# Kernel tuning notes

Hardware: AMD Instinct MI355X
Metric: run time of the kernel (lower is better)

Reference implementation:

```python
import jax, jax.numpy as jnp
import numpy as np

D_MODEL, N_HEADS, D_K, D_V, D_FF, N_LAYERS = 512, 8, 64, 64, 2048, 6
NEG = -1e9
EPS = 1e-5


def layernorm(x):
    # nn.LayerNorm(d_model) created fresh each call: weight=1, bias=0
    mu = jnp.mean(x, axis=-1, keepdims=True)
    var = jnp.var(x, axis=-1, keepdims=True)
    return (x - mu) * jax.lax.rsqrt(var + EPS)


def sinusoidal_pe(seq_len, d_model, dtype=jnp.float32):
    pos = np.arange(seq_len)[:, None].astype(np.float64)
    div = np.exp(np.arange(0, d_model, 2).astype(np.float64) * (-np.log(10000.0) / d_model))
    pe = np.zeros((seq_len, d_model))
    pe[:, 0::2] = np.sin(pos * div)
    pe[:, 1::2] = np.cos(pos * div)
    return jnp.asarray(pe, dtype=dtype)


def mha(q_in, k_in, v_in, mask, Wq, Wk, Wv, Wo):
    # q_in: [B,Lq,D]; k_in/v_in: [B,Lk,D]; mask: [B,Lq,Lk] bool (True = masked)
    B, Lq, _ = q_in.shape
    Lk = k_in.shape[1]
    Q = (q_in @ Wq).reshape(B, Lq, N_HEADS, D_K).transpose(0, 2, 1, 3)
    K = (k_in @ Wk).reshape(B, Lk, N_HEADS, D_K).transpose(0, 2, 1, 3)
    V = (v_in @ Wv).reshape(B, Lk, N_HEADS, D_V).transpose(0, 2, 1, 3)
    scores = jnp.einsum('bhqd,bhkd->bhqk', Q, K) / jnp.sqrt(jnp.asarray(D_K, q_in.dtype))
    scores = jnp.where(mask[:, None, :, :], jnp.asarray(NEG, scores.dtype), scores)
    attn = jax.nn.softmax(scores, axis=-1)
    ctx = jnp.einsum('bhqk,bhkd->bhqd', attn, V)
    ctx = ctx.transpose(0, 2, 1, 3).reshape(B, Lq, N_HEADS * D_V)
    return layernorm(ctx @ Wo + q_in)


def setup_inputs() -> dict:
    key = jax.random.key(0)
    ks = jax.random.split(key, 16)
    B, T, S, V = 8, 1024, 1024, 32000
    s = 0.02
    inp = {
        'dec_inputs': jax.random.randint(ks[0], (B, T), 0, V),
        'enc_inputs': jax.random.randint(ks[1], (B, S), 0, V),
        'enc_outputs': jax.random.normal(ks[2], (B, S, D_MODEL), jnp.float32),
        'emb': jax.random.normal(ks[3], (V, D_MODEL), jnp.float32) * s,
        'Wq_self': jax.random.normal(ks[4], (N_LAYERS, D_MODEL, N_HEADS * D_K), jnp.float32) * s,
        'Wk_self': jax.random.normal(ks[5], (N_LAYERS, D_MODEL, N_HEADS * D_K), jnp.float32) * s,
        'Wv_self': jax.random.normal(ks[6], (N_LAYERS, D_MODEL, N_HEADS * D_V), jnp.float32) * s,
        'Wo_self': jax.random.normal(ks[7], (N_LAYERS, N_HEADS * D_V, D_MODEL), jnp.float32) * s,
        'Wq_cross': jax.random.normal(ks[8], (N_LAYERS, D_MODEL, N_HEADS * D_K), jnp.float32) * s,
        'Wk_cross': jax.random.normal(ks[9], (N_LAYERS, D_MODEL, N_HEADS * D_K), jnp.float32) * s,
        'Wv_cross': jax.random.normal(ks[10], (N_LAYERS, D_MODEL, N_HEADS * D_V), jnp.float32) * s,
        'Wo_cross': jax.random.normal(ks[11], (N_LAYERS, N_HEADS * D_V, D_MODEL), jnp.float32) * s,
        'W1': jax.random.normal(ks[12], (N_LAYERS, D_MODEL, D_FF), jnp.float32) * s,
        'W2': jax.random.normal(ks[13], (N_LAYERS, D_FF, D_MODEL), jnp.float32) * s,
    }
    return inp


def reference(dec_inputs, enc_inputs, enc_outputs, emb, Wq_self, Wk_self, Wv_self, Wo_self,
              Wq_cross, Wk_cross, Wv_cross, Wo_cross, W1, W2):
    B, T = dec_inputs.shape
    S = enc_inputs.shape[1]
    # embedding with padding_idx=0 (row 0 forced to zero)
    emb_eff = emb.at[0].set(0.0)
    x = emb_eff[dec_inputs] + sinusoidal_pe(T, D_MODEL, emb.dtype)[None, :, :]
    # masks: True = masked
    pad_self = (dec_inputs == 0)[:, None, :]                       # [B,1,T]
    causal = jnp.triu(jnp.ones((T, T), bool), k=1)[None, :, :]     # [1,T,T]
    self_mask = pad_self | causal                                  # [B,T,T]
    enc_mask = jnp.broadcast_to((enc_inputs == 0)[:, None, :], (B, T, S))

    def layer(x, p):
        wqs, wks, wvs, wos, wqc, wkc, wvc, woc, w1, w2 = p
        x = mha(x, x, x, self_mask, wqs, wks, wvs, wos)
        x = mha(x, enc_outputs, enc_outputs, enc_mask, wqc, wkc, wvc, woc)
        h = jax.nn.relu(x @ w1) @ w2
        return layernorm(h + x), None

    params = (Wq_self, Wk_self, Wv_self, Wo_self, Wq_cross, Wk_cross, Wv_cross, Wo_cross, W1, W2)
    x, _ = jax.lax.scan(layer, x, params)
    return x
```

## Files before the change

kernel.cpp:

```cpp
#include <hip/hip_runtime.h>
#include <hip/hip_bf16.h>

#define DMODEL 512
#define NH     8
#define DHEAD  64
#define DFF    2048
#define NLAYER 6
#define BB     8
#define TT     1024
#define NTOK   (BB*TT)
#define ACTE   ((size_t)NTOK*DMODEL)

typedef __bf16  bf16x8  __attribute__((ext_vector_type(8)));
typedef float   float4v __attribute__((ext_vector_type(4)));
typedef short   short4v __attribute__((ext_vector_type(4)));
typedef short   short8v __attribute__((ext_vector_type(8)));

__device__ __forceinline__ unsigned short f2bf(float f) {
    __hip_bfloat16 h = __float2bfloat16(f);
    return *reinterpret_cast<unsigned short*>(&h);
}

__device__ __forceinline__ void gl_lds16(const void* g, void* l) {
    __builtin_amdgcn_global_load_lds((const __attribute__((address_space(1))) void*)g,
                                     (__attribute__((address_space(3))) void*)l, 16, 0, 0);
}
__device__ __forceinline__ void wave_order() { __builtin_amdgcn_wave_barrier(); }

struct Tr8Args {
    const float* src[8];
    unsigned short* dst[8];
    int dstL[8];
    int rowOff[8];
};
__global__ __launch_bounds__(256) void transpose8_kernel(Tr8Args a)
{
    __shared__ float tile[64][65];
    const int type = blockIdx.z / 6, lyr = blockIdx.z % 6;
    const float* src = a.src[type] + (size_t)lyr * 512 * 512;
    unsigned short* dst = a.dst[type] + (size_t)lyr * a.dstL[type];
    const int rowOff = a.rowOff[type];
    const int k0 = blockIdx.x * 64, n0 = blockIdx.y * 64;
    const int tid = threadIdx.x;
#pragma unroll
    for (int rep = 0; rep < 16; ++rep) {
        int idx = rep * 256 + tid;
        int r = idx >> 6, c = idx & 63;
        tile[r][c] = src[(size_t)(k0 + r) * 512 + n0 + c];
    }
    __syncthreads();
#pragma unroll
    for (int rep = 0; rep < 16; ++rep) {
        int idx = rep * 256 + tid;
        int r = idx >> 6, c = idx & 63;
        dst[(size_t)(rowOff + n0 + r) * 512 + k0 + c] = f2bf(tile[c][r]);
    }
}

__global__ __launch_bounds__(256) void transpose_conv_kernel(
    const float* __restrict__ W, unsigned short* __restrict__ Wt, int K, int N,
    size_t dstL, int rowOff)
{
    __shared__ float tile[64][65];
    const float* src = W + (size_t)blockIdx.z * K * N;
    unsigned short* dst = Wt + (size_t)blockIdx.z * dstL;
    const int k0 = blockIdx.x * 64, n0 = blockIdx.y * 64;
    const int tid = threadIdx.x;
#pragma unroll
    for (int rep = 0; rep < 16; ++rep) {
        int idx = rep * 256 + tid;
        int r = idx >> 6, c = idx & 63;
        tile[r][c] = src[(size_t)(k0 + r) * N + n0 + c];
    }
    __syncthreads();
#pragma unroll
    for (int rep = 0; rep < 16; ++rep) {
        int idx = rep * 256 + tid;
        int r = idx >> 6, c = idx & 63;
        dst[(size_t)(rowOff + n0 + r) * K + k0 + c] = f2bf(tile[c][r]);
    }
}

__global__ __launch_bounds__(256) void conv_bf16_kernel(
    const float* __restrict__ in, unsigned short* __restrict__ o)
{
    int i = (blockIdx.x * 256 + threadIdx.x) * 4;
    float4v v = *(const float4v*)(in + i);
    short4v w;
    w[0] = (short)f2bf(v[0]); w[1] = (short)f2bf(v[1]);
    w[2] = (short)f2bf(v[2]); w[3] = (short)f2bf(v[3]);
    *(short4v*)(o + i) = w;
}

__global__ __launch_bounds__(256) void embed_kernel(
    const int* __restrict__ dec, const float* __restrict__ emb,
    unsigned short* __restrict__ xb)
{
    const int row = blockIdx.x;
    const int t = row & (TT - 1);
    const int tid = threadIdx.x;
    const int tok = dec[row];
#pragma unroll
    for (int rep = 0; rep < 2; ++rep) {
        int c = tid + rep * 256;
        float e = (tok != 0) ? emb[(size_t)tok * DMODEL + c] : 0.f;
        int j = c >> 1;
        float freq = __expf(-(float)(2 * j) * (9.210340371976184f / 512.f));
        float ang = (float)t * freq;
        float pe = (c & 1) ? cosf(ang) : sinf(ang);
        xb[(size_t)row * DMODEL + c] = f2bf(e + pe);
    }
}

__global__ __launch_bounds__(256) void add_ln2(
    const float* __restrict__ t, unsigned short* __restrict__ xb,
    float* __restrict__ xout)
{
    const int lane = threadIdx.x & 63;
    const int row = blockIdx.x * 4 + (threadIdx.x >> 6);
    const size_t idx = (size_t)row * DMODEL + lane * 8;
    float4v t0 = *(const float4v*)(t + idx);
    float4v t1 = *(const float4v*)(t + idx + 4);
    float4v u0 = *(const float4v*)(t + ACTE + idx);
    float4v u1 = *(const float4v*)(t + ACTE + idx + 4);
    bf16x8 rb = *(const bf16x8*)(xb + idx);
    float v[8];
#pragma unroll
    for (int k = 0; k < 4; ++k) {
        v[k] = t0[k] + u0[k] + (float)rb[k];
        v[4 + k] = t1[k] + u1[k] + (float)rb[4 + k];
    }
    float s = 0.f, sq = 0.f;
#pragma unroll
    for (int k = 0; k < 8; ++k) { s += v[k]; sq += v[k] * v[k]; }
#pragma unroll
    for (int o = 1; o < 64; o <<= 1) { s += __shfl_xor(s, o); sq += __shfl_xor(sq, o); }
    float mu = s * (1.f / 512.f);
    float var = sq * (1.f / 512.f) - mu * mu;
    float rstd = rsqrtf(var + 1e-5f);
    if (xout) {
        float4v y0, y1;
#pragma unroll
        for (int k = 0; k < 4; ++k) { y0[k] = (v[k] - mu) * rstd; y1[k] = (v[4 + k] - mu) * rstd; }
        *(float4v*)(xout + idx) = y0;
        *(float4v*)(xout + idx + 4) = y1;
    } else {
        short8v w;
#pragma unroll
        for (int k = 0; k < 8; ++k) w[k] = (short)f2bf((v[k] - mu) * rstd);
        *(short8v*)(xb + idx) = w;
    }
}

template <int EPI, int SPLITK = 1>
__global__ __launch_bounds__(256) void gemm_bt(
    const unsigned short* __restrict__ A,
    const unsigned short* __restrict__ Bt,
    float* __restrict__ Cf,
    unsigned short* __restrict__ Cb,
    int M, int N, int K)
{
    __shared__ __attribute__((aligned(16))) short As[128 * 32];
    __shared__ __attribute__((aligned(16))) short Bs[128 * 32];
    const int tid = threadIdx.x;
    const int lane = tid & 63, wv = tid >> 6;
    const int quad = lane >> 4, l15 = lane & 15;
    const int m0 = blockIdx.x * 128, n0 = blockIdx.y * 128;
    const int wm = wv & 1, wn = wv >> 1;

    float4v acc[4][4];
#pragma unroll
    for (int i = 0; i < 4; ++i)
#pragma unroll
        for (int j = 0; j < 4; ++j) acc[i][j] = (float4v){0.f, 0.f, 0.f, 0.f};

    const int Kc = K / SPLITK;
    const int kbeg = (SPLITK > 1) ? (int)blockIdx.z * Kc : 0;
    for (int k0 = kbeg; k0 < kbeg + Kc; k0 += 32) {
#pragma unroll
        for (int i = 0; i < 2; ++i) {
            const int inst = wv * 2 + i;
            const int row = inst * 16 + (lane >> 2);
            const int cb = (lane & 3) ^ ((row >> 1) & 3);
            gl_lds16(A + (size_t)(m0 + row) * K + k0 + cb * 8, (char*)As + inst * 1024);
            gl_lds16(Bt + (size_t)(n0 + row) * K + k0 + cb * 8, (char*)Bs + inst * 1024);
        }
        __syncthreads();
        bf16x8 a[4], b[4];
#pragma unroll
        for (int i = 0; i < 4; ++i) {
            const int r = wm * 64 + i * 16 + l15;
            const int st = quad ^ ((r >> 1) & 3);
            a[i] = *(const bf16x8*)&As[r * 32 + st * 8];
        }
#pragma unroll
        for (int j = 0; j < 4; ++j) {
            const int r = wn * 64 + j * 16 + l15;
            const int st = quad ^ ((r >> 1) & 3);
            b[j] = *(const bf16x8*)&Bs[r * 32 + st * 8];
        }
#pragma unroll
        for (int i = 0; i < 4; ++i)
#pragma unroll
            for (int j = 0; j < 4; ++j)
                acc[i][j] = __builtin_amdgcn_mfma_f32_16x16x32_bf16(a[i], b[j], acc[i][j], 0, 0, 0);
        __syncthreads();
    }

    const size_t zoff = (SPLITK > 1) ? (size_t)blockIdx.z * ACTE : 0;
#pragma unroll
    for (int i = 0; i < 4; ++i) {
        const int row_base = m0 + wm * 64 + i * 16 + quad * 4;
#pragma unroll
        for (int j = 0; j < 4; ++j) {
            const int col = n0 + wn * 64 + j * 16 + l15;
#pragma unroll
            for (int r = 0; r < 4; ++r) {
                const int row = row_base + r;
                const float v = acc[i][j][r];
                if (EPI == 0) {
                    Cf[zoff + (size_t)row * N + col] = v;
                } else if (EPI == 1) {
                    Cb[(size_t)row * N + col] = f2bf(fmaxf(v, 0.f));
                } else if (EPI == 2) {
                    const int which = col >> 9;
                    const int b_ = row >> 10, t = row & (TT - 1);
                    const int h = (col >> 6) & 7, d = col & 63;
                    Cb[(size_t)which * ACTE + (((size_t)(b_ * NH + h)) * TT + t) * DHEAD + d] = f2bf(v);
                } else {
                    const int layer = col >> 10, which = (col >> 9) & 1;
                    const int b_ = row >> 10, t = row & (TT - 1);
                    const int h = (col >> 6) & 7, d = col & 63;
                    Cb[(size_t)(layer * 2 + which) * ACTE +
                       (((size_t)(b_ * NH + h)) * TT + t) * DHEAD + d] = f2bf(v);
                }
            }
        }
    }
}

template <bool CAUSAL>
__global__ __launch_bounds__(256) void attn_kernel(
    const unsigned short* __restrict__ Q,
    const unsigned short* __restrict__ Kb,
    const unsigned short* __restrict__ Vb,
    const int* __restrict__ tokens,
    unsigned short* __restrict__ ctx)
{
    __shared__ __attribute__((aligned(16))) short Ks[64 * 64];
    __shared__ __attribute__((aligned(16))) short Vt[64 * 64];
    __shared__ __attribute__((aligned(16))) short Pl[4][16 * 72];
    __shared__ __attribute__((aligned(16))) float alphas[4][16];
    __shared__ int kmask[64];

    const int tid = threadIdx.x, lane = tid & 63, wv = tid >> 6;
    const int quad = lane >> 4, l15 = lane & 15;
    const int p = blockIdx.x;
    const int bh = blockIdx.y;
    const int b = bh >> 3, h = bh & 7;
    const size_t kvbase = (size_t)bh * TT * DHEAD;

    const int qt0 = p;
    const int qt1 = CAUSAL ? (15 - p) : (p + 8);
    const int qg0 = qt0 * 64 + wv * 16 + l15;
    const int qg1 = qt1 * 64 + wv * 16 + l15;

    const bf16x8 qa0 = *(const bf16x8*)&Q[kvbase + (size_t)qg0 * DHEAD + quad * 8];
    const bf16x8 qa1 = *(const bf16x8*)&Q[kvbase + (size_t)qg0 * DHEAD + 32 + quad * 8];
    const bf16x8 qb0 = *(const bf16x8*)&Q[kvbase + (size_t)qg1 * DHEAD + quad * 8];
    const bf16x8 qb1 = *(const bf16x8*)&Q[kvbase + (size_t)qg1 * DHEAD + 32 + quad * 8];

    float4v O0[4], O1[4];
#pragma unroll
    for (int j = 0; j < 4; ++j) { O0[j] = (float4v){0.f,0.f,0.f,0.f}; O1[j] = (float4v){0.f,0.f,0.f,0.f}; }
    float m0_ = -INFINITY, l0_ = 0.f, m1_ = -INFINITY, l1_ = 0.f;

    int kt = 0;
    auto process = [&](const bf16x8& qf0, const bf16x8& qf1, int qg,
                       float& m, float& l, float4v* O) {
        float4v st[4];
#pragma unroll
        for (int i = 0; i < 4; ++i) {
            const int row = i * 16 + l15;
            const int s0 = quad ^ (row & 7);
            const int s1 = (4 + quad) ^ (row & 7);
            bf16x8 kf0 = *(const bf16x8*)&Ks[row * 64 + s0 * 8];
            bf16x8 kf1 = *(const bf16x8*)&Ks[row * 64 + s1 * 8];
            float4v z = (float4v){0.f, 0.f, 0.f, 0.f};
            z = __builtin_amdgcn_mfma_f32_16x16x32_bf16(kf0, qf0, z, 0, 0, 0);
            z = __builtin_amdgcn_mfma_f32_16x16x32_bf16(kf1, qf1, z, 0, 0, 0);
            st[i] = z;
        }
        float sv[16], smax = -INFINITY;
#pragma unroll
        for (int i = 0; i < 4; ++i)
#pragma unroll
            for (int r = 0; r < 4; ++r) {
                const int key_local = i * 16 + quad * 4 + r;
                const int key_g = kt * 64 + key_local;
                bool msk = (kmask[key_local] != 0) || (CAUSAL && key_g > qg);
                float s = msk ? -1e9f : st[i][r] * 0.125f;
                sv[i * 4 + r] = s;
                smax = fmaxf(smax, s);
            }
        smax = fmaxf(smax, __shfl_xor(smax, 16));
        smax = fmaxf(smax, __shfl_xor(smax, 32));
        const float mnew = fmaxf(m, smax);
        const float alpha = __expf(m - mnew);
        float tsum = 0.f;
#pragma unroll
        for (int i = 0; i < 16; ++i) { float pv = __expf(sv[i] - mnew); sv[i] = pv; tsum += pv; }
        tsum += __shfl_xor(tsum, 16);
        tsum += __shfl_xor(tsum, 32);
        l = l * alpha + tsum;
        m = mnew;
        wave_order();
#pragma unroll
        for (int i = 0; i < 4; ++i) {
            short4v pw;
#pragma unroll
            for (int r = 0; r < 4; ++r) pw[r] = (short)f2bf(sv[i * 4 + r]);
            *(short4v*)&Pl[wv][l15 * 72 + i * 16 + quad * 4] = pw;
        }
        if (lane < 16) alphas[wv][lane] = alpha;
        wave_order();
        const float4v aw = *(const float4v*)&alphas[wv][quad * 4];
        const bf16x8 p0 = *(const bf16x8*)&Pl[wv][l15 * 72 + quad * 8];
        const bf16x8 p1 = *(const bf16x8*)&Pl[wv][l15 * 72 + 32 + quad * 8];
#pragma unroll
        for (int j = 0; j < 4; ++j) {
            const int row = j * 16 + l15;
            const int s0 = quad ^ (row & 7);
            const int s1 = (4 + quad) ^ (row & 7);
            bf16x8 v0f = *(const bf16x8*)&Vt[row * 64 + s0 * 8];
            bf16x8 v1f = *(const bf16x8*)&Vt[row * 64 + s1 * 8];
            float4v o = O[j] * aw;
            o = __builtin_amdgcn_mfma_f32_16x16x32_bf16(p0, v0f, o, 0, 0, 0);
            o = __builtin_amdgcn_mfma_f32_16x16x32_bf16(p1, v1f, o, 0, 0, 0);
            O[j] = o;
        }
    };

    const int nkt = CAUSAL ? (qt1 + 1) : 16;
    for (kt = 0; kt < nkt; ++kt) {
        __syncthreads();
#pragma unroll
        for (int i = 0; i < 2; ++i) {
            const int inst = wv * 2 + i;
            const int row = inst * 8 + (lane >> 3);
            const int cb = (lane & 7) ^ (row & 7);
            gl_lds16(Kb + kvbase + (size_t)(kt * 64 + row) * DHEAD + cb * 8,
                     (char*)Ks + inst * 1024);
        }
        {
            const int key0 = (lane & 31) * 2;
            const int d0 = (lane >> 5) * 8 + wv * 16;
            const unsigned short* vp = Vb + kvbase + (size_t)(kt * 64 + key0) * DHEAD + d0;
            short8v r0 = *(const short8v*)vp;
            short8v r1 = *(const short8v*)(vp + DHEAD);
            const int kc = key0 >> 3, ko = key0 & 7;
#pragma unroll
            for (int j = 0; j < 8; ++j) {
                const int d = d0 + j;
                unsigned pk = (unsigned)(unsigned short)r0[j] |
                              ((unsigned)(unsigned short)r1[j] << 16);
                *(unsigned*)&Vt[d * 64 + ((kc ^ (d & 7)) << 3) + ko] = pk;
            }
        }
        if (tid < 64) kmask[tid] = (tokens[(size_t)b * TT + kt * 64 + tid] == 0);
        __syncthreads();

        if (!CAUSAL || kt <= qt0) process(qa0, qa1, qg0, m0_, l0_, O0);
        process(qb0, qb1, qg1, m1_, l1_, O1);
    }

    auto finalize = [&](float l, float4v* O, int qt) {
        wave_order();
        if (lane < 16) alphas[wv][lane] = l;
        wave_order();
        const float4v lw = *(const float4v*)&alphas[wv][quad * 4];
#pragma unroll
        for (int j = 0; j < 4; ++j)
#pragma unroll
            for (int r = 0; r < 4; ++r) {
                const int qrow = qt * 64 + wv * 16 + quad * 4 + r;
                ctx[((size_t)b * TT + qrow) * DMODEL + h * DHEAD + j * 16 + l15] =
                    f2bf(O[j][r] / lw[r]);
            }
    };
    finalize(l0_, O0, qt0);
    finalize(l1_, O1, qt1);
}

extern "C" void kernel_launch(void* const* d_in, const int* in_sizes, int n_in,
                              void* d_out, int out_size, void* d_ws, size_t ws_size,
                              hipStream_t stream)
{
    const int* dec = (const int*)d_in[0];
    const int* enc = (const int*)d_in[1];
    const float* enc_out = (const float*)d_in[2];
    const float* emb = (const float*)d_in[3];
    const float* Wq_s = (const float*)d_in[4];
    const float* Wk_s = (const float*)d_in[5];
    const float* Wv_s = (const float*)d_in[6];
    const float* Wo_s = (const float*)d_in[7];
    const float* Wq_c = (const float*)d_in[8];
    const float* Wk_c = (const float*)d_in[9];
    const float* Wv_c = (const float*)d_in[10];
    const float* Wo_c = (const float*)d_in[11];
    const float* W1 = (const float*)d_in[12];
    const float* W2 = (const float*)d_in[13];
    float* out = (float*)d_out;

    char* p = (char*)d_ws;
    auto carve = [&](size_t bytes) -> char* {
        char* r = p;
        p += (bytes + 255) & ~(size_t)255;
        return r;
    };
    unsigned short* xb   = (unsigned short*)carve(ACTE * 2);
    float* tmp1          = (float*)carve(2 * ACTE * 4);
    unsigned short* qkvb = (unsigned short*)carve(3 * ACTE * 2);
    unsigned short* ctxb = (unsigned short*)carve(ACTE * 2);
    unsigned short* encb = (unsigned short*)carve(ACTE * 2);
    unsigned short* h1   = (unsigned short*)carve((size_t)NTOK * DFF * 2);
    unsigned short* wqkvT = (unsigned short*)carve((size_t)NLAYER * 1536 * 512 * 2);
    unsigned short* woT   = (unsigned short*)carve((size_t)NLAYER * 512 * 512 * 2);
    unsigned short* wqcT  = (unsigned short*)carve((size_t)NLAYER * 512 * 512 * 2);
    unsigned short* wkvcT = (unsigned short*)carve((size_t)NLAYER * 1024 * 512 * 2);
    unsigned short* wocT  = (unsigned short*)carve((size_t)NLAYER * 512 * 512 * 2);
    unsigned short* w1T   = (unsigned short*)carve((size_t)NLAYER * 2048 * 512 * 2);
    unsigned short* w2T   = (unsigned short*)carve((size_t)NLAYER * 512 * 2048 * 2);
    const size_t used = (size_t)(p - (char*)d_ws);
    const bool pre = (used + 12 * ACTE * 2 + 256) <= ws_size;
    unsigned short* KVc = pre ? (unsigned short*)carve(12 * ACTE * 2) : nullptr;

    Tr8Args ta;
    ta.src[0] = Wq_s; ta.dst[0] = wqkvT; ta.dstL[0] = 1536 * 512; ta.rowOff[0] = 0;
    ta.src[1] = Wk_s; ta.dst[1] = wqkvT; ta.dstL[1] = 1536 * 512; ta.rowOff[1] = 512;
    ta.src[2] = Wv_s; ta.dst[2] = wqkvT; ta.dstL[2] = 1536 * 512; ta.rowOff[2] = 1024;
    ta.src[3] = Wo_s; ta.dst[3] = woT;   ta.dstL[3] = 512 * 512;  ta.rowOff[3] = 0;
    ta.src[4] = Wq_c; ta.dst[4] = wqcT;  ta.dstL[4] = 512 * 512;  ta.rowOff[4] = 0;
    ta.src[5] = Wk_c; ta.dst[5] = wkvcT; ta.dstL[5] = 1024 * 512; ta.rowOff[5] = 0;
    ta.src[6] = Wv_c; ta.dst[6] = wkvcT; ta.dstL[6] = 1024 * 512; ta.rowOff[6] = 512;
    ta.src[7] = Wo_c; ta.dst[7] = wocT;  ta.dstL[7] = 512 * 512;  ta.rowOff[7] = 0;
    transpose8_kernel<<<dim3(8, 8, 48), 256, 0, stream>>>(ta);
    transpose_conv_kernel<<<dim3(8, 32, NLAYER), 256, 0, stream>>>(W1, w1T, 512, 2048, (size_t)2048 * 512, 0);
    transpose_conv_kernel<<<dim3(32, 8, NLAYER), 256, 0, stream>>>(W2, w2T, 2048, 512, (size_t)512 * 2048, 0);
    conv_bf16_kernel<<<(int)(ACTE / 1024), 256, 0, stream>>>(enc_out, encb);
    embed_kernel<<<NTOK, 256, 0, stream>>>(dec, emb, xb);

    if (pre)
        gemm_bt<3><<<dim3(64, 48), 256, 0, stream>>>(encb, wkvcT, nullptr, KVc, NTOK, 6144, 512);

    for (int lyr = 0; lyr < NLAYER; ++lyr) {
        const unsigned short* wqkv = wqkvT + (size_t)lyr * 1536 * 512;
        const unsigned short* wo   = woT + (size_t)lyr * 512 * 512;
        const unsigned short* wqc  = wqcT + (size_t)lyr * 512 * 512;
        const unsigned short* wkvc = wkvcT + (size_t)lyr * 1024 * 512;
        const unsigned short* woc  = wocT + (size_t)lyr * 512 * 512;
        const unsigned short* w1   = w1T + (size_t)lyr * 2048 * 512;
        const unsigned short* w2   = w2T + (size_t)lyr * 512 * 2048;

        gemm_bt<2><<<dim3(64, 12), 256, 0, stream>>>(xb, wqkv, nullptr, qkvb, NTOK, 1536, 512);
        attn_kernel<true><<<dim3(8, BB * NH), 256, 0, stream>>>(
            qkvb, qkvb + ACTE, qkvb + 2 * ACTE, dec, ctxb);
        gemm_bt<0, 2><<<dim3(64, 4, 2), 256, 0, stream>>>(ctxb, wo, tmp1, nullptr, NTOK, 512, 512);
        add_ln2<<<NTOK / 4, 256, 0, stream>>>(tmp1, xb, nullptr);

        gemm_bt<2><<<dim3(64, 4), 256, 0, stream>>>(xb, wqc, nullptr, qkvb, NTOK, 512, 512);
        const unsigned short* Kc;
        if (pre) {
            Kc = KVc + (size_t)lyr * 2 * ACTE;
        } else {
            gemm_bt<2><<<dim3(64, 8), 256, 0, stream>>>(encb, wkvc, nullptr, qkvb + ACTE, NTOK, 1024, 512);
            Kc = qkvb + ACTE;
        }
        attn_kernel<false><<<dim3(8, BB * NH), 256, 0, stream>>>(
            qkvb, Kc, Kc + ACTE, enc, ctxb);
        gemm_bt<0, 2><<<dim3(64, 4, 2), 256, 0, stream>>>(ctxb, woc, tmp1, nullptr, NTOK, 512, 512);
        add_ln2<<<NTOK / 4, 256, 0, stream>>>(tmp1, xb, nullptr);

        gemm_bt<1><<<dim3(64, 16), 256, 0, stream>>>(xb, w1, nullptr, h1, NTOK, 2048, 512);
        gemm_bt<0, 2><<<dim3(64, 4, 2), 256, 0, stream>>>(h1, w2, tmp1, nullptr, NTOK, 512, 2048);
        add_ln2<<<NTOK / 4, 256, 0, stream>>>(tmp1, xb, (lyr == NLAYER - 1) ? out : nullptr);
    }
    (void)in_sizes; (void)n_in; (void)out_size;
}
```

Baseline: 1.755 ms.

## Double-buffer K/V tiles in attention and precompute key padding mask via ballot

The attention kernel now double-buffers the K and V LDS tiles. It prefetches the next key tile (K through global_load_lds, V into registers) while the current tile is processed, which cuts the loop to one __syncthreads per iteration instead of two. The padding mask is built with a wave ballot into a 64-bit mask that also folds in the causal mask, replacing per-element shared-memory lookups. The 1/sqrt(d) scale moves into the Q projection epilogue. Dropping the wave barriers around the per-wave P/alpha LDS round-trip relies on in-order LDS access within a wave, and the double buffers increase LDS usage.

```diff
diff --git a/kernel.cpp b/kernel.cpp
--- a/kernel.cpp
+++ b/kernel.cpp
@@ -25,7 +25,6 @@
     __builtin_amdgcn_global_load_lds((const __attribute__((address_space(1))) void*)g,
                                      (__attribute__((address_space(3))) void*)l, 16, 0, 0);
 }
-__device__ __forceinline__ void wave_order() { __builtin_amdgcn_wave_barrier(); }
 
 struct Tr8Args {
     const float* src[8];
@@ -224,9 +223,10 @@
                     Cb[(size_t)row * N + col] = f2bf(fmaxf(v, 0.f));
                 } else if (EPI == 2) {
                     const int which = col >> 9;
+                    const float sc = (which == 0) ? 0.125f : 1.f;
                     const int b_ = row >> 10, t = row & (TT - 1);
                     const int h = (col >> 6) & 7, d = col & 63;
-                    Cb[(size_t)which * ACTE + (((size_t)(b_ * NH + h)) * TT + t) * DHEAD + d] = f2bf(v);
+                    Cb[(size_t)which * ACTE + (((size_t)(b_ * NH + h)) * TT + t) * DHEAD + d] = f2bf(v * sc);
                 } else {
                     const int layer = col >> 10, which = (col >> 9) & 1;
                     const int b_ = row >> 10, t = row & (TT - 1);
@@ -247,11 +247,10 @@
     const int* __restrict__ tokens,
     unsigned short* __restrict__ ctx)
 {
-    __shared__ __attribute__((aligned(16))) short Ks[64 * 64];
-    __shared__ __attribute__((aligned(16))) short Vt[64 * 64];
-    __shared__ __attribute__((aligned(16))) short Pl[4][16 * 72];
-    __shared__ __attribute__((aligned(16))) float alphas[4][16];
-    __shared__ int kmask[64];
+    __shared__ __attribute__((aligned(16))) short Ks[2][64 * 64];
+    __shared__ __attribute__((aligned(16))) short Vt[2][64 * 64];
+    __shared__ __attribute__((aligned(16))) short Pl[2][4][16 * 72];
+    __shared__ __attribute__((aligned(16))) float alph[2][4][16];
 
     const int tid = threadIdx.x, lane = tid & 63, wv = tid >> 6;
     const int quad = lane >> 4, l15 = lane & 15;
@@ -275,31 +274,63 @@
     for (int j = 0; j < 4; ++j) { O0[j] = (float4v){0.f,0.f,0.f,0.f}; O1[j] = (float4v){0.f,0.f,0.f,0.f}; }
     float m0_ = -INFINITY, l0_ = 0.f, m1_ = -INFINITY, l1_ = 0.f;
 
+    const int key0 = (lane & 31) * 2;
+    const int d0 = (lane >> 5) * 8 + wv * 16;
+    auto stageK = [&](int kt, int buf) {
+#pragma unroll
+        for (int i = 0; i < 2; ++i) {
+            const int inst = wv * 2 + i;
+            const int row = inst * 8 + (lane >> 3);
+            const int cb = (lane & 7) ^ (row & 7);
+            gl_lds16(Kb + kvbase + (size_t)(kt * 64 + row) * DHEAD + cb * 8,
+                     (char*)Ks[buf] + inst * 1024);
+        }
+    };
+    auto loadV = [&](int kt, short8v& r0, short8v& r1) {
+        const unsigned short* vp = Vb + kvbase + (size_t)(kt * 64 + key0) * DHEAD + d0;
+        r0 = *(const short8v*)vp;
+        r1 = *(const short8v*)(vp + DHEAD);
+    };
+    auto writeV = [&](int buf, const short8v& r0, const short8v& r1) {
+        const int kc = key0 >> 3, ko = key0 & 7;
+#pragma unroll
+        for (int j = 0; j < 8; ++j) {
+            const int d = d0 + j;
+            unsigned pk = (unsigned)(unsigned short)r0[j] |
+                          ((unsigned)(unsigned short)r1[j] << 16);
+            *(unsigned*)&Vt[buf][d * 64 + ((kc ^ (d & 7)) << 3) + ko] = pk;
+        }
+    };
+
     int kt = 0;
-    auto process = [&](const bf16x8& qf0, const bf16x8& qf1, int qg,
-                       float& m, float& l, float4v* O) {
+    auto process = [&](int ch, const bf16x8& qf0, const bf16x8& qf1, int qg,
+                       float& m, float& l, float4v* O,
+                       int cur, unsigned long long kbits) {
         float4v st[4];
 #pragma unroll
         for (int i = 0; i < 4; ++i) {
             const int row = i * 16 + l15;
             const int s0 = quad ^ (row & 7);
             const int s1 = (4 + quad) ^ (row & 7);
-            bf16x8 kf0 = *(const bf16x8*)&Ks[row * 64 + s0 * 8];
-            bf16x8 kf1 = *(const bf16x8*)&Ks[row * 64 + s1 * 8];
+            bf16x8 kf0 = *(const bf16x8*)&Ks[cur][row * 64 + s0 * 8];
+            bf16x8 kf1 = *(const bf16x8*)&Ks[cur][row * 64 + s1 * 8];
             float4v z = (float4v){0.f, 0.f, 0.f, 0.f};
             z = __builtin_amdgcn_mfma_f32_16x16x32_bf16(kf0, qf0, z, 0, 0, 0);
             z = __builtin_amdgcn_mfma_f32_16x16x32_bf16(kf1, qf1, z, 0, 0, 0);
             st[i] = z;
         }
+        unsigned long long mask = kbits;
+        if (CAUSAL && kt * 64 + 63 > qg) {
+            const int qcol = qg & 63;
+            mask |= (qcol == 63) ? 0ull : (~0ull << (qcol + 1));
+        }
         float sv[16], smax = -INFINITY;
 #pragma unroll
         for (int i = 0; i < 4; ++i)
 #pragma unroll
             for (int r = 0; r < 4; ++r) {
-                const int key_local = i * 16 + quad * 4 + r;
-                const int key_g = kt * 64 + key_local;
-                bool msk = (kmask[key_local] != 0) || (CAUSAL && key_g > qg);
-                float s = msk ? -1e9f : st[i][r] * 0.125f;
+                const int kl = i * 16 + quad * 4 + r;
+                float s = ((mask >> kl) & 1ull) ? -1e9f : st[i][r];
                 sv[i * 4 + r] = s;
                 smax = fmaxf(smax, s);
             }
@@ -314,26 +345,24 @@
         tsum += __shfl_xor(tsum, 32);
         l = l * alpha + tsum;
         m = mnew;
-        wave_order();
 #pragma unroll
         for (int i = 0; i < 4; ++i) {
             short4v pw;
 #pragma unroll
             for (int r = 0; r < 4; ++r) pw[r] = (short)f2bf(sv[i * 4 + r]);
-            *(short4v*)&Pl[wv][l15 * 72 + i * 16 + quad * 4] = pw;
-        }
-        if (lane < 16) alphas[wv][lane] = alpha;
-        wave_order();
-        const float4v aw = *(const float4v*)&alphas[wv][quad * 4];
-        const bf16x8 p0 = *(const bf16x8*)&Pl[wv][l15 * 72 + quad * 8];
-        const bf16x8 p1 = *(const bf16x8*)&Pl[wv][l15 * 72 + 32 + quad * 8];
+            *(short4v*)&Pl[ch][wv][l15 * 72 + i * 16 + quad * 4] = pw;
+        }
+        if (lane < 16) alph[ch][wv][lane] = alpha;
+        const float4v aw = *(const float4v*)&alph[ch][wv][quad * 4];
+        const bf16x8 p0 = *(const bf16x8*)&Pl[ch][wv][l15 * 72 + quad * 8];
+        const bf16x8 p1 = *(const bf16x8*)&Pl[ch][wv][l15 * 72 + 32 + quad * 8];
 #pragma unroll
         for (int j = 0; j < 4; ++j) {
             const int row = j * 16 + l15;
             const int s0 = quad ^ (row & 7);
             const int s1 = (4 + quad) ^ (row & 7);
-            bf16x8 v0f = *(const bf16x8*)&Vt[row * 64 + s0 * 8];
-            bf16x8 v1f = *(const bf16x8*)&Vt[row * 64 + s1 * 8];
+            bf16x8 v0f = *(const bf16x8*)&Vt[cur][row * 64 + s0 * 8];
+            bf16x8 v1f = *(const bf16x8*)&Vt[cur][row * 64 + s1 * 8];
             float4v o = O[j] * aw;
             o = __builtin_amdgcn_mfma_f32_16x16x32_bf16(p0, v0f, o, 0, 0, 0);
             o = __builtin_amdgcn_mfma_f32_16x16x32_bf16(p1, v1f, o, 0, 0, 0);
@@ -342,43 +371,41 @@
     };
 
     const int nkt = CAUSAL ? (qt1 + 1) : 16;
+
+    stageK(0, 0);
+    {
+        short8v v0a, v0b;
+        loadV(0, v0a, v0b);
+        writeV(0, v0a, v0b);
+    }
+    int tok_cur = tokens[(size_t)b * TT + lane];
+    __syncthreads();
+
+    short8v vn0, vn1;
+    int tok_next = 0;
     for (kt = 0; kt < nkt; ++kt) {
+        const int cur = kt & 1, nxt = cur ^ 1;
+        const bool more = (kt + 1 < nkt);
+        if (more) {
+            stageK(kt + 1, nxt);
+            loadV(kt + 1, vn0, vn1);
+            tok_next = tokens[(size_t)b * TT + (kt + 1) * 64 + lane];
+        }
+        const unsigned long long kbits = __ballot(tok_cur == 0);
+
+        if (!CAUSAL || kt <= qt0) process(0, qa0, qa1, qg0, m0_, l0_, O0, cur, kbits);
+        process(1, qb0, qb1, qg1, m1_, l1_, O1, cur, kbits);
+
+        if (more) {
+            writeV(nxt, vn0, vn1);
+            tok_cur = tok_next;
+        }
         __syncthreads();
-#pragma unroll
-        for (int i = 0; i < 2; ++i) {
-            const int inst = wv * 2 + i;
-            const int row = inst * 8 + (lane >> 3);
-            const int cb = (lane & 7) ^ (row & 7);
-            gl_lds16(Kb + kvbase + (size_t)(kt * 64 + row) * DHEAD + cb * 8,
-                     (char*)Ks + inst * 1024);
-        }
-        {
-            const int key0 = (lane & 31) * 2;
-            const int d0 = (lane >> 5) * 8 + wv * 16;
-            const unsigned short* vp = Vb + kvbase + (size_t)(kt * 64 + key0) * DHEAD + d0;
-            short8v r0 = *(const short8v*)vp;
-            short8v r1 = *(const short8v*)(vp + DHEAD);
-            const int kc = key0 >> 3, ko = key0 & 7;
-#pragma unroll
-            for (int j = 0; j < 8; ++j) {
-                const int d = d0 + j;
-                unsigned pk = (unsigned)(unsigned short)r0[j] |
-                              ((unsigned)(unsigned short)r1[j] << 16);
-                *(unsigned*)&Vt[d * 64 + ((kc ^ (d & 7)) << 3) + ko] = pk;
-            }
-        }
-        if (tid < 64) kmask[tid] = (tokens[(size_t)b * TT + kt * 64 + tid] == 0);
-        __syncthreads();
-
-        if (!CAUSAL || kt <= qt0) process(qa0, qa1, qg0, m0_, l0_, O0);
-        process(qb0, qb1, qg1, m1_, l1_, O1);
-    }
-
-    auto finalize = [&](float l, float4v* O, int qt) {
-        wave_order();
-        if (lane < 16) alphas[wv][lane] = l;
-        wave_order();
-        const float4v lw = *(const float4v*)&alphas[wv][quad * 4];
+    }
+
+    auto finalize = [&](int ch, float l, float4v* O, int qt) {
+        if (lane < 16) alph[ch][wv][lane] = l;
+        const float4v lw = *(const float4v*)&alph[ch][wv][quad * 4];
 #pragma unroll
         for (int j = 0; j < 4; ++j)
 #pragma unroll
@@ -388,8 +415,8 @@
                     f2bf(O[j][r] / lw[r]);
             }
     };
-    finalize(l0_, O0, qt0);
-    finalize(l1_, O1, qt1);
+    finalize(0, l0_, O0, qt0);
+    finalize(1, l1_, O1, qt1);
 }
 
 extern "C" void kernel_launch(void* const* d_in, const int* in_sizes, int n_in,
```

After: 1.689 ms. -3.8%, faster.
